# Kernel optimization log

Measured on AMD Instinct MI355X. Metric: run time of the kernel, lower is better.

The kernel has to match this reference:

```python
import jax, jax.numpy as jnp
import numpy as np

N, E = 50000, 800000
IN_DIM, H_DIM, OUT_DIM, EDGE_DIM, HEADS = 128, 128, 112, 8, 1
NEG_SLOPE = 0.2
BN_EPS = 1e-5


def _gat_layer(x, src, dst, edge_att, W, a_src, a_dst, We, a_edge, bias):
    """PyG GATConv (concat=False, edge_dim used for attention only)."""
    H, C = a_src.shape  # heads, out channels
    xs = (x @ W).reshape(-1, H, C)            # [N,H,C]
    ef = (edge_att @ We).reshape(-1, H, C)    # [E,H,C]
    al_src = jnp.einsum('nhc,hc->nh', xs, a_src)   # [N,H]
    al_dst = jnp.einsum('nhc,hc->nh', xs, a_dst)   # [N,H]
    al_edge = jnp.einsum('ehc,hc->eh', ef, a_edge) # [E,H]
    alpha = al_src[src] + al_dst[dst] + al_edge    # [E,H]
    alpha = jnp.where(alpha > 0, alpha, NEG_SLOPE * alpha)  # leaky_relu(0.2)
    # segment softmax over incoming edges of each dst node
    m = jax.lax.stop_gradient(jax.ops.segment_max(alpha, dst, num_segments=N))
    ex = jnp.exp(alpha - m[dst])
    den = jax.ops.segment_sum(ex, dst, num_segments=N)
    att = ex / den[dst]                       # [E,H]
    msg = xs[src] * att[:, :, None]           # [E,H,C] gather + weight
    out = jax.ops.segment_sum(msg, dst, num_segments=N)  # scatter-add [N,H,C]
    return out.mean(axis=1) + bias            # concat=False -> head mean


def _batchnorm(h, gamma, beta):
    mu = h.mean(axis=0)
    var = h.var(axis=0)
    return gamma * (h - mu) * jax.lax.rsqrt(var + BN_EPS) + beta


def setup_inputs() -> dict:
    key = jax.random.key(0)
    ks = jax.random.split(key, 20)
    s = 0.1
    inp = {
        'x': jax.random.normal(ks[0], (N, IN_DIM), dtype=jnp.float32),
        'edge_index': jax.random.randint(ks[1], (2, E), 0, N, dtype=jnp.int32),
        'edge_att': jax.random.normal(ks[2], (E, EDGE_DIM), dtype=jnp.float32),
        # layer 0: IN_DIM -> H_DIM
        'W0': s * jax.random.normal(ks[3], (IN_DIM, HEADS * H_DIM), dtype=jnp.float32),
        'a_src0': s * jax.random.normal(ks[4], (HEADS, H_DIM), dtype=jnp.float32),
        'a_dst0': s * jax.random.normal(ks[5], (HEADS, H_DIM), dtype=jnp.float32),
        'We0': s * jax.random.normal(ks[6], (EDGE_DIM, HEADS * H_DIM), dtype=jnp.float32),
        'a_edge0': s * jax.random.normal(ks[7], (HEADS, H_DIM), dtype=jnp.float32),
        'b0': jnp.zeros((H_DIM,), dtype=jnp.float32),
        # layer 1: H_DIM -> OUT_DIM
        'W1': s * jax.random.normal(ks[8], (H_DIM, HEADS * OUT_DIM), dtype=jnp.float32),
        'a_src1': s * jax.random.normal(ks[9], (HEADS, OUT_DIM), dtype=jnp.float32),
        'a_dst1': s * jax.random.normal(ks[10], (HEADS, OUT_DIM), dtype=jnp.float32),
        'We1': s * jax.random.normal(ks[11], (EDGE_DIM, HEADS * OUT_DIM), dtype=jnp.float32),
        'a_edge1': s * jax.random.normal(ks[12], (HEADS, OUT_DIM), dtype=jnp.float32),
        'b1': jnp.zeros((OUT_DIM,), dtype=jnp.float32),
        # batchnorms
        'bn_g': jnp.ones((H_DIM,), dtype=jnp.float32),
        'bn_b': jnp.zeros((H_DIM,), dtype=jnp.float32),
        'bnf_g': jnp.ones((OUT_DIM,), dtype=jnp.float32),
        'bnf_b': jnp.zeros((OUT_DIM,), dtype=jnp.float32),
    }
    return inp


def reference(x, edge_index, edge_att,
              W0, a_src0, a_dst0, We0, a_edge0, b0,
              W1, a_src1, a_dst1, We1, a_edge1, b1,
              bn_g, bn_b, bnf_g, bnf_b):
    src, dst = edge_index[0], edge_index[1]
    h = _gat_layer(x, src, dst, edge_att, W0, a_src0, a_dst0, We0, a_edge0, b0)
    h = _batchnorm(h, bn_g, bn_b)
    h = jax.nn.relu(h)
    # dropout is a no-op in eval; omitted for a deterministic reference
    h = _gat_layer(h, src, dst, edge_att, W1, a_src1, a_dst1, We1, a_edge1, b1)
    h = _batchnorm(h, bnf_g, bnf_b)
    return h
```

## Files before the change

kernel.cpp:

```cpp
#include <hip/hip_runtime.h>
#include <math.h>

#define NN 50000
#define NPAD 50048
#define NE 800000
#define SCAN_B 256
#define SCAN_NBLK ((NN + SCAN_B - 1) / SCAN_B)
#define AGG_NBLK 2048

typedef __attribute__((ext_vector_type(8))) short bf16x8;
typedef __attribute__((ext_vector_type(4))) float f32x4;
typedef __attribute__((ext_vector_type(8))) unsigned short u16x8;

__device__ __forceinline__ unsigned short f2bf(float x) {
    unsigned u = __float_as_uint(x);
    u += 0x7fffu + ((u >> 16) & 1);
    return (unsigned short)(u >> 16);
}
__device__ __forceinline__ float bf2f(unsigned short h) {
    return __uint_as_float(((unsigned)h) << 16);
}

__global__ void k_init_cvt(int* __restrict__ deg, float* __restrict__ stats,
                           const float* __restrict__ We0, const float* __restrict__ ae0,
                           const float* __restrict__ We1, const float* __restrict__ ae1,
                           float* __restrict__ ve,
                           const float* __restrict__ W0, const float* __restrict__ W1,
                           unsigned short* __restrict__ Wth0, unsigned short* __restrict__ Wtl0,
                           unsigned short* __restrict__ Wth1, unsigned short* __restrict__ Wtl1)
{
    int idx = blockIdx.x * 256 + threadIdx.x;
    if (idx < NN) deg[idx] = 0;
    if (idx < 512) stats[idx] = 0.f;
    if (idx < 128 * 128) {
        int k = idx / 128, c = idx % 128;
        float v = W0[idx];
        unsigned short hi = f2bf(v);
        Wth0[c * 128 + k] = hi;
        Wtl0[c * 128 + k] = f2bf(v - bf2f(hi));
    } else if (idx < 128 * 128 + 128 * 112) {
        int i2 = idx - 128 * 128;
        int k = i2 / 112, c = i2 % 112;
        float v = W1[i2];
        unsigned short hi = f2bf(v);
        Wth1[c * 128 + k] = hi;
        Wtl1[c * 128 + k] = f2bf(v - bf2f(hi));
    }
    if (blockIdx.x == gridDim.x - 1) {
        int j = threadIdx.x;
        if (j < 8) {
            float s = 0.f;
            for (int c = 0; c < 128; ++c) s += We0[j * 128 + c] * ae0[c];
            ve[j] = s;
        } else if (j < 16) {
            int jj = j - 8;
            float s = 0.f;
            for (int c = 0; c < 112; ++c) s += We1[jj * 112 + c] * ae1[c];
            ve[8 + jj] = s;
        }
    }
}

__global__ void k_deg(const int* __restrict__ dst, int* __restrict__ deg,
                      int* __restrict__ rank, int E_)
{
    int e = blockIdx.x * blockDim.x + threadIdx.x;
    if (e < E_) rank[e] = atomicAdd(&deg[dst[e]], 1);
}

__global__ void k_scan1(const int* __restrict__ deg, int* __restrict__ partial)
{
    __shared__ int sm[SCAN_B];
    int t = threadIdx.x;
    int idx = blockIdx.x * SCAN_B + t;
    sm[t] = (idx < NN) ? deg[idx] : 0;
    __syncthreads();
    #pragma unroll
    for (int off = SCAN_B / 2; off > 0; off >>= 1) {
        if (t < off) sm[t] += sm[t + off];
        __syncthreads();
    }
    if (t == 0) partial[blockIdx.x] = sm[0];
}

__global__ void k_scan3(const int* __restrict__ deg, const int* __restrict__ partial,
                        int* __restrict__ rp)
{
    __shared__ int sm[SCAN_B];
    __shared__ int pbase;
    int t = threadIdx.x;
    int pv = (t < SCAN_NBLK && t < blockIdx.x) ? partial[t] : 0;
    sm[t] = pv;
    __syncthreads();
    #pragma unroll
    for (int off = SCAN_B / 2; off > 0; off >>= 1) {
        if (t < off) sm[t] += sm[t + off];
        __syncthreads();
    }
    if (t == 0) pbase = sm[0];
    __syncthreads();
    int idx = blockIdx.x * SCAN_B + t;
    int v = (idx < NN) ? deg[idx] : 0;
    sm[t] = v;
    __syncthreads();
    #pragma unroll
    for (int off = 1; off < SCAN_B; off <<= 1) {
        int u = (t >= off) ? sm[t - off] : 0;
        __syncthreads();
        sm[t] += u;
        __syncthreads();
    }
    int excl = pbase + ((t == 0) ? 0 : sm[t - 1]);
    if (idx < NN) rp[idx] = excl;
    if (idx == NN - 1) rp[NN] = excl + v;
}

__global__ void k_csr_fill_l0(const int* __restrict__ src, const int* __restrict__ dst,
                              const float* __restrict__ eatt, const float* __restrict__ ve,
                              const int* __restrict__ rp, const int* __restrict__ rank,
                              const float* __restrict__ als, const float* __restrict__ ald,
                              uint4* __restrict__ pk, int E_)
{
    int e = blockIdx.x * blockDim.x + threadIdx.x;
    if (e >= E_) return;
    const float4* ea = reinterpret_cast<const float4*>(eatt + (size_t)e * 8);
    float4 e0 = ea[0], e1 = ea[1];
    float a0 = e0.x * ve[0] + e0.y * ve[1] + e0.z * ve[2] + e0.w * ve[3]
             + e1.x * ve[4] + e1.y * ve[5] + e1.z * ve[6] + e1.w * ve[7];
    float a1 = e0.x * ve[8] + e0.y * ve[9] + e0.z * ve[10] + e0.w * ve[11]
             + e1.x * ve[12] + e1.y * ve[13] + e1.z * ve[14] + e1.w * ve[15];
    int s = src[e], d = dst[e];
    float av = als[s] + ald[d] + a0;
    av = av > 0.f ? av : 0.2f * av;
    float ex0 = __expf(av);
    int pos = rp[d] + rank[e];
    uint4 rec;
    rec.x = (unsigned)s;
    rec.y = __float_as_uint(ex0);
    rec.z = __float_as_uint(a1);
    rec.w = 0u;
    pk[pos] = rec;
}

template<int COLS, bool BN_IN>
__launch_bounds__(256, 2)
__global__ void k_gemm_mfma(const float* __restrict__ A,
                            const unsigned short* __restrict__ Wth,
                            const unsigned short* __restrict__ Wtl,
                            unsigned short* __restrict__ out,
                            const float* __restrict__ a_src, const float* __restrict__ a_dst,
                            float* __restrict__ als, float* __restrict__ ald,
                            const float* __restrict__ bsum, const float* __restrict__ bsq,
                            const float* __restrict__ gamma, const float* __restrict__ beta)
{
    constexpr int NT = COLS / 16;
    __shared__ unsigned short sBh[COLS * 128];
    __shared__ unsigned short sBl[COLS * 128];
    __shared__ float scN[128], shN[128];

    int wv = threadIdx.x >> 6;
    int lane = threadIdx.x & 63;
    int r0 = blockIdx.x * 64 + wv * 16;
    int m = lane & 15;
    int quad = lane >> 4;
    int arow = r0 + m;
    int rc = (arow < NN) ? arow : NN - 1;
    const float* pa = A + (size_t)rc * 128 + quad * 8;

    float4 av[8];
    #pragma unroll
    for (int ks = 0; ks < 4; ++ks) {
        av[2 * ks]     = *reinterpret_cast<const float4*>(pa + ks * 32);
        av[2 * ks + 1] = *reinterpret_cast<const float4*>(pa + ks * 32 + 4);
    }

    constexpr int CH = COLS * 128 * 2 / 16;
    for (int i = threadIdx.x; i < CH; i += 256) {
        unsigned o = (unsigned)i * 16u;
        unsigned d = o ^ (((o >> 8) & 7u) << 4);
        *reinterpret_cast<uint4*>(reinterpret_cast<char*>(sBh) + d) =
            *reinterpret_cast<const uint4*>(reinterpret_cast<const char*>(Wth) + o);
        *reinterpret_cast<uint4*>(reinterpret_cast<char*>(sBl) + d) =
            *reinterpret_cast<const uint4*>(reinterpret_cast<const char*>(Wtl) + o);
    }
    if (BN_IN) {
        if (threadIdx.x < 128) {
            int k = threadIdx.x;
            float invn = 1.0f / (float)NN;
            float mean = bsum[k] * invn;
            float var  = bsq[k] * invn - mean * mean;
            float sc = gamma[k] * rsqrtf(var + 1e-5f);
            scN[k] = sc;
            shN[k] = beta[k] - mean * sc;
        }
    }
    __syncthreads();

    f32x4 acc[NT];
    #pragma unroll
    for (int t = 0; t < NT; ++t) acc[t] = f32x4{0.f, 0.f, 0.f, 0.f};

    unsigned swz = ((unsigned)(m & 7)) << 4;

    #pragma unroll
    for (int ks = 0; ks < 4; ++ks) {
        float4 v0 = av[2 * ks], v1 = av[2 * ks + 1];
        float vv[8] = {v0.x, v0.y, v0.z, v0.w, v1.x, v1.y, v1.z, v1.w};
        int kb = ks * 32 + quad * 8;
        bf16x8 ah, al;
        #pragma unroll
        for (int jj = 0; jj < 8; ++jj) {
            float f = vv[jj];
            if (BN_IN) f = fmaxf(f * scN[kb + jj] + shN[kb + jj], 0.f);
            unsigned short hi = f2bf(f);
            ah[jj] = (short)hi;
            al[jj] = (short)f2bf(f - bf2f(hi));
        }
        #pragma unroll
        for (int t = 0; t < NT; ++t) {
            int c = t * 16 + m;
            unsigned b = ((unsigned)c * 256u + (unsigned)ks * 64u + (unsigned)quad * 16u) ^ swz;
            bf16x8 bh = *reinterpret_cast<const bf16x8*>(reinterpret_cast<const char*>(sBh) + b);
            bf16x8 bl = *reinterpret_cast<const bf16x8*>(reinterpret_cast<const char*>(sBl) + b);
            acc[t] = __builtin_amdgcn_mfma_f32_16x16x32_bf16(ah, bh, acc[t], 0, 0, 0);
            acc[t] = __builtin_amdgcn_mfma_f32_16x16x32_bf16(al, bh, acc[t], 0, 0, 0);
            acc[t] = __builtin_amdgcn_mfma_f32_16x16x32_bf16(ah, bl, acc[t], 0, 0, 0);
        }
    }

    float p[4] = {0.f, 0.f, 0.f, 0.f}, q[4] = {0.f, 0.f, 0.f, 0.f};
    #pragma unroll
    for (int t = 0; t < NT; ++t) {
        int c = t * 16 + m;
        float asv = a_src[c], adv = a_dst[c];
        #pragma unroll
        for (int rI = 0; rI < 4; ++rI) {
            float v = acc[t][rI];
            int row = r0 + quad * 4 + rI;
            if (row < NN) out[(size_t)row * COLS + c] = f2bf(v);
            p[rI] += v * asv;
            q[rI] += v * adv;
        }
    }
    #pragma unroll
    for (int rI = 0; rI < 4; ++rI) {
        #pragma unroll
        for (int off = 1; off <= 8; off <<= 1) {
            p[rI] += __shfl_xor(p[rI], off);
            q[rI] += __shfl_xor(q[rI], off);
        }
    }
    if (m == 0) {
        #pragma unroll
        for (int rI = 0; rI < 4; ++rI) {
            int row = r0 + quad * 4 + rI;
            if (row < NN) { als[row] = p[rI]; ald[row] = q[rI]; }
        }
    }
}

__global__ void k_logit1(const int* __restrict__ rp, const uint4* __restrict__ pk,
                         const float* __restrict__ als, const float* __restrict__ ald,
                         uint2* __restrict__ pe)
{
    int ql = threadIdx.x & 15;
    int w = blockIdx.x * 16 + (threadIdx.x >> 4);
    if (w >= NN) return;
    int beg = rp[w], end = rp[w + 1];
    float aldv = ald[w];
    for (int p = beg + ql; p < end; p += 16) {
        uint4 r = pk[p];
        float a = als[r.x] + aldv + __uint_as_float(r.z);
        a = a > 0.f ? a : 0.2f * a;
        uint2 o;
        o.x = r.x;
        o.y = __float_as_uint(__expf(a));
        pe[p] = o;
    }
}

template<int COLS, int RSTRIDE>
__global__ void k_aggregate(const int* __restrict__ rp, const uint2* __restrict__ pe,
                            const unsigned short* __restrict__ xs, float* __restrict__ out,
                            float* __restrict__ psum, float* __restrict__ psq)
{
    __shared__ float sS[16 * 128], sQ[16 * 128];
    int ql = threadIdx.x & 15;
    int wq = threadIdx.x >> 4;
    int col = ql * 8;
    bool act = (col < COLS);
    int qid = blockIdx.x * 16 + wq;
    float bs[8] = {0.f,0.f,0.f,0.f,0.f,0.f,0.f,0.f};
    float bq[8] = {0.f,0.f,0.f,0.f,0.f,0.f,0.f,0.f};

    for (int w = qid; w < NN; w += AGG_NBLK * 16) {
        int beg = rp[w], end = rp[w + 1];
        float acc[8] = {0.f,0.f,0.f,0.f,0.f,0.f,0.f,0.f};
        float den = 0.f;
        int j = beg;
        for (; j + 4 <= end; j += 4) {
            uint2 r0 = pe[(size_t)(j    ) * RSTRIDE];
            uint2 r1 = pe[(size_t)(j + 1) * RSTRIDE];
            uint2 r2 = pe[(size_t)(j + 2) * RSTRIDE];
            uint2 r3 = pe[(size_t)(j + 3) * RSTRIDE];
            float e0 = __uint_as_float(r0.y);
            float e1 = __uint_as_float(r1.y);
            float e2 = __uint_as_float(r2.y);
            float e3 = __uint_as_float(r3.y);
            den += (e0 + e1) + (e2 + e3);
            if (act) {
                u16x8 u0 = *reinterpret_cast<const u16x8*>(xs + (size_t)r0.x * COLS + col);
                u16x8 u1 = *reinterpret_cast<const u16x8*>(xs + (size_t)r1.x * COLS + col);
                u16x8 u2 = *reinterpret_cast<const u16x8*>(xs + (size_t)r2.x * COLS + col);
                u16x8 u3 = *reinterpret_cast<const u16x8*>(xs + (size_t)r3.x * COLS + col);
                #pragma unroll
                for (int k = 0; k < 8; ++k)
                    acc[k] += (e0 * bf2f(u0[k]) + e1 * bf2f(u1[k]))
                            + (e2 * bf2f(u2[k]) + e3 * bf2f(u3[k]));
            }
        }
        if (j < end) {
            bool v1 = j + 1 < end;
            bool v2 = j + 2 < end;
            bool v3 = j + 3 < end;
            uint2 r0 = pe[(size_t)j * RSTRIDE];
            uint2 r1 = v1 ? pe[(size_t)(j + 1) * RSTRIDE] : uint2{0u, 0u};
            uint2 r2 = v2 ? pe[(size_t)(j + 2) * RSTRIDE] : uint2{0u, 0u};
            uint2 r3 = v3 ? pe[(size_t)(j + 3) * RSTRIDE] : uint2{0u, 0u};
            float e0 = __uint_as_float(r0.y);
            float e1 = __uint_as_float(r1.y);
            float e2 = __uint_as_float(r2.y);
            float e3 = __uint_as_float(r3.y);
            den += (e0 + e1) + (e2 + e3);
            if (act) {
                u16x8 u0 = *reinterpret_cast<const u16x8*>(xs + (size_t)r0.x * COLS + col);
                #pragma unroll
                for (int k = 0; k < 8; ++k) acc[k] += e0 * bf2f(u0[k]);
                if (v1) {
                    u16x8 u1 = *reinterpret_cast<const u16x8*>(xs + (size_t)r1.x * COLS + col);
                    #pragma unroll
                    for (int k = 0; k < 8; ++k) acc[k] += e1 * bf2f(u1[k]);
                }
                if (v2) {
                    u16x8 u2 = *reinterpret_cast<const u16x8*>(xs + (size_t)r2.x * COLS + col);
                    #pragma unroll
                    for (int k = 0; k < 8; ++k) acc[k] += e2 * bf2f(u2[k]);
                }
                if (v3) {
                    u16x8 u3 = *reinterpret_cast<const u16x8*>(xs + (size_t)r3.x * COLS + col);
                    #pragma unroll
                    for (int k = 0; k < 8; ++k) acc[k] += e3 * bf2f(u3[k]);
                }
            }
        }
        float inv = (end > beg) ? 1.f / den : 0.f;
        if (act) {
            float o[8];
            #pragma unroll
            for (int k = 0; k < 8; ++k) {
                o[k] = acc[k] * inv;
                bs[k] += o[k];
                bq[k] += o[k] * o[k];
            }
            f32x4 o0 = {o[0], o[1], o[2], o[3]};
            f32x4 o1 = {o[4], o[5], o[6], o[7]};
            __builtin_nontemporal_store(o0, reinterpret_cast<f32x4*>(out + (size_t)w * COLS + col));
            __builtin_nontemporal_store(o1, reinterpret_cast<f32x4*>(out + (size_t)w * COLS + col + 4));
        }
    }
    #pragma unroll
    for (int k = 0; k < 8; ++k) {
        sS[wq * 128 + col + k] = act ? bs[k] : 0.f;
        sQ[wq * 128 + col + k] = act ? bq[k] : 0.f;
    }
    __syncthreads();
    int t = threadIdx.x;
    if (t < 128) {
        float s = 0.f, s2 = 0.f;
        #pragma unroll
        for (int r = 0; r < 16; ++r) { s += sS[r * 128 + t]; s2 += sQ[r * 128 + t]; }
        psum[(size_t)blockIdx.x * 128 + t] = s;
        psq [(size_t)blockIdx.x * 128 + t] = s2;
    }
}

__global__ void k_bn_stats2(const float* __restrict__ psum, const float* __restrict__ psq,
                            float* __restrict__ sums, float* __restrict__ sqs)
{
    int t = threadIdx.x;
    int c = t & 127;
    constexpr int ROWS = AGG_NBLK / 128;
    const float* sp = (t < 128) ? psum : psq;
    float s = 0.f;
    #pragma unroll 4
    for (int i = 0; i < ROWS; ++i)
        s += sp[(size_t)(blockIdx.x * ROWS + i) * 128 + c];
    unsafeAtomicAdd(((t < 128) ? sums : sqs) + c, s);
}

template<int COLS>
__global__ void k_bn_apply(const float* __restrict__ in, float* __restrict__ out,
                           const float* __restrict__ sums, const float* __restrict__ sqs,
                           const float* __restrict__ gamma, const float* __restrict__ beta,
                           int n)
{
    int idx = blockIdx.x * blockDim.x + threadIdx.x;
    if (idx >= n * COLS) return;
    int c = idx % COLS;
    float invn = 1.0f / (float)n;
    float mean = sums[c] * invn;
    float var  = sqs[c] * invn - mean * mean;
    float sc = gamma[c] * rsqrtf(var + 1e-5f);
    float sh = beta[c] - mean * sc;
    out[idx] = in[idx] * sc + sh;
}

extern "C" void kernel_launch(void* const* d_in, const int* in_sizes, int n_in,
                              void* d_out, int out_size, void* d_ws, size_t ws_size,
                              hipStream_t stream)
{
    const float* x    = (const float*)d_in[0];
    const int*   eidx = (const int*)d_in[1];
    const float* eatt = (const float*)d_in[2];
    const float* W0   = (const float*)d_in[3];
    const float* as0  = (const float*)d_in[4];
    const float* ad0  = (const float*)d_in[5];
    const float* We0  = (const float*)d_in[6];
    const float* ae0  = (const float*)d_in[7];
    const float* W1   = (const float*)d_in[9];
    const float* as1  = (const float*)d_in[10];
    const float* ad1  = (const float*)d_in[11];
    const float* We1  = (const float*)d_in[12];
    const float* ae1  = (const float*)d_in[13];
    const float* bng  = (const float*)d_in[15];
    const float* bnb  = (const float*)d_in[16];
    const float* bnfg = (const float*)d_in[17];
    const float* bnfb = (const float*)d_in[18];

    const int N = NN, E = NE;
    const int* src = eidx;
    const int* dst = eidx + E;

    float* ws = (float*)d_ws;
    size_t off = 0;
    unsigned short* xs0b = (unsigned short*)(ws + off); off += (size_t)N * 64;
    float* h   = ws + off;      off += (size_t)N * 128;
    unsigned short* xs1b = (unsigned short*)(ws + off); off += (size_t)N * 56;
    int*   rp   = (int*)(ws + off);     off += N + 2;
    int*   rank = (int*)(ws + off);     off += E;
    int*   deg  = (int*)(ws + off);     off += N;
    float* als0 = ws + off;     off += N;
    float* ald0 = ws + off;     off += N;
    float* als1 = ws + off;     off += N;
    float* ald1 = ws + off;     off += N;
    float* stats = ws + off;    off += 512;
    float* ve = ws + off;       off += 16;
    int*   partial = (int*)(ws + off);  off += SCAN_NBLK;
    float* psum = ws + off;     off += (size_t)AGG_NBLK * 128;
    float* psq  = ws + off;     off += (size_t)AGG_NBLK * 128;
    unsigned short* Wth0 = (unsigned short*)(ws + off); off += 128 * 64;
    unsigned short* Wtl0 = (unsigned short*)(ws + off); off += 128 * 64;
    unsigned short* Wth1 = (unsigned short*)(ws + off); off += 112 * 64;
    unsigned short* Wtl1 = (unsigned short*)(ws + off); off += 112 * 64;
    float* out1 = h;

    uint4* pk  = (uint4*)d_out;
    uint2* pe1 = (uint2*)((char*)d_out + (size_t)E * 16);

    float* sum0 = stats;
    float* sq0  = stats + 128;
    float* sum1 = stats + 256;
    float* sq1  = stats + 384;

    k_init_cvt<<<(N + 255) / 256, 256, 0, stream>>>(deg, stats, We0, ae0, We1, ae1, ve,
                                                    W0, W1, Wth0, Wtl0, Wth1, Wtl1);

    k_deg<<<(E + 255) / 256, 256, 0, stream>>>(dst, deg, rank, E);
    k_scan1<<<SCAN_NBLK, SCAN_B, 0, stream>>>(deg, partial);
    k_scan3<<<SCAN_NBLK, SCAN_B, 0, stream>>>(deg, partial, rp);

    k_gemm_mfma<128, false><<<NPAD / 64, 256, 0, stream>>>(x, Wth0, Wtl0, xs0b,
                                                           as0, ad0, als0, ald0,
                                                           nullptr, nullptr, nullptr, nullptr);
    k_csr_fill_l0<<<(E + 255) / 256, 256, 0, stream>>>(src, dst, eatt, ve, rp, rank,
                                                       als0, ald0, pk, E);
    k_aggregate<128, 2><<<AGG_NBLK, 256, 0, stream>>>(rp, (const uint2*)pk, xs0b, h, psum, psq);
    k_bn_stats2<<<128, 256, 0, stream>>>(psum, psq, sum0, sq0);

    k_gemm_mfma<112, true><<<NPAD / 64, 256, 0, stream>>>(h, Wth1, Wtl1, xs1b,
                                                          as1, ad1, als1, ald1,
                                                          sum0, sq0, bng, bnb);
    k_logit1<<<(N + 15) / 16, 256, 0, stream>>>(rp, pk, als1, ald1, pe1);
    k_aggregate<112, 1><<<AGG_NBLK, 256, 0, stream>>>(rp, pe1, xs1b, out1, psum, psq);
    k_bn_stats2<<<128, 256, 0, stream>>>(psum, psq, sum1, sq1);
    k_bn_apply<112><<<(N * 112 + 255) / 256, 256, 0, stream>>>(out1, (float*)d_out, sum1, sq1, bnfg, bnfb, N);
}
```

Baseline: 339.8 us.

## Pack edge records into 8 bytes and unroll aggregation by eight

Each CSR edge record shrinks from a 16-byte uint4 to an 8-byte uint2. The source index goes in the low 16 bits, the layer-1 edge logit as bf16 in the high 16 bits, and the exp value in the second word. The fill kernel now handles two edges per thread with vectorized index loads. The aggregate kernel is unrolled to eight edges per iteration and now reads a contiguous record stream. The aggregate block count goes up, and rank/deg/pe1 are aliased onto workspace buffers that are already dead, so scratch no longer lives in the output buffer. This cuts scatter and gather bytes, but relies on N fitting in 16 bits and stores the edge logit at bf16 precision.

Measured after the change: 345.9 us. About the same (+1.8%).

```diff
diff --git a/kernel.cpp b/kernel.cpp
--- a/kernel.cpp
+++ b/kernel.cpp
@@ -6,7 +6,7 @@
 #define NE 800000
 #define SCAN_B 256
 #define SCAN_NBLK ((NN + SCAN_B - 1) / SCAN_B)
-#define AGG_NBLK 2048
+#define AGG_NBLK 3200
 
 typedef __attribute__((ext_vector_type(8))) short bf16x8;
 typedef __attribute__((ext_vector_type(4))) float f32x4;
@@ -119,27 +119,40 @@
                               const float* __restrict__ eatt, const float* __restrict__ ve,
                               const int* __restrict__ rp, const int* __restrict__ rank,
                               const float* __restrict__ als, const float* __restrict__ ald,
-                              uint4* __restrict__ pk, int E_)
-{
-    int e = blockIdx.x * blockDim.x + threadIdx.x;
+                              uint2* __restrict__ pk, int E_)
+{
+    int i = blockIdx.x * blockDim.x + threadIdx.x;
+    int e = i * 2;
     if (e >= E_) return;
+    int2 ss = *reinterpret_cast<const int2*>(src + e);
+    int2 dd = *reinterpret_cast<const int2*>(dst + e);
+    int2 rr = *reinterpret_cast<const int2*>(rank + e);
     const float4* ea = reinterpret_cast<const float4*>(eatt + (size_t)e * 8);
-    float4 e0 = ea[0], e1 = ea[1];
-    float a0 = e0.x * ve[0] + e0.y * ve[1] + e0.z * ve[2] + e0.w * ve[3]
-             + e1.x * ve[4] + e1.y * ve[5] + e1.z * ve[6] + e1.w * ve[7];
-    float a1 = e0.x * ve[8] + e0.y * ve[9] + e0.z * ve[10] + e0.w * ve[11]
-             + e1.x * ve[12] + e1.y * ve[13] + e1.z * ve[14] + e1.w * ve[15];
-    int s = src[e], d = dst[e];
-    float av = als[s] + ald[d] + a0;
-    av = av > 0.f ? av : 0.2f * av;
-    float ex0 = __expf(av);
-    int pos = rp[d] + rank[e];
-    uint4 rec;
-    rec.x = (unsigned)s;
-    rec.y = __float_as_uint(ex0);
-    rec.z = __float_as_uint(a1);
-    rec.w = 0u;
-    pk[pos] = rec;
+    float4 ea0 = ea[0], ea1 = ea[1], ea2 = ea[2], ea3 = ea[3];
+
+    float a0x = ea0.x * ve[0] + ea0.y * ve[1] + ea0.z * ve[2] + ea0.w * ve[3]
+              + ea1.x * ve[4] + ea1.y * ve[5] + ea1.z * ve[6] + ea1.w * ve[7];
+    float a1x = ea0.x * ve[8] + ea0.y * ve[9] + ea0.z * ve[10] + ea0.w * ve[11]
+              + ea1.x * ve[12] + ea1.y * ve[13] + ea1.z * ve[14] + ea1.w * ve[15];
+    float a0y = ea2.x * ve[0] + ea2.y * ve[1] + ea2.z * ve[2] + ea2.w * ve[3]
+              + ea3.x * ve[4] + ea3.y * ve[5] + ea3.z * ve[6] + ea3.w * ve[7];
+    float a1y = ea2.x * ve[8] + ea2.y * ve[9] + ea2.z * ve[10] + ea2.w * ve[11]
+              + ea3.x * ve[12] + ea3.y * ve[13] + ea3.z * ve[14] + ea3.w * ve[15];
+
+    int p0 = rp[dd.x] + rr.x;
+    int p1 = rp[dd.y] + rr.y;
+    float lx = als[ss.x] + ald[dd.x] + a0x;
+    float ly = als[ss.y] + ald[dd.y] + a0y;
+    lx = lx > 0.f ? lx : 0.2f * lx;
+    ly = ly > 0.f ? ly : 0.2f * ly;
+
+    uint2 r0, r1;
+    r0.x = (unsigned)ss.x | ((unsigned)f2bf(a1x) << 16);
+    r0.y = __float_as_uint(__expf(lx));
+    r1.x = (unsigned)ss.y | ((unsigned)f2bf(a1y) << 16);
+    r1.y = __float_as_uint(__expf(ly));
+    pk[p0] = r0;
+    pk[p1] = r1;
 }
 
 template<int COLS, bool BN_IN>
@@ -259,9 +272,9 @@
     }
 }
 
-__global__ void k_logit1(const int* __restrict__ rp, const uint4* __restrict__ pk,
+__global__ void k_logit1(const int* __restrict__ rp, const uint2* __restrict__ pk,
                          const float* __restrict__ als, const float* __restrict__ ald,
-                         uint2* __restrict__ pe)
+                         uint2* __restrict__ pe1)
 {
     int ql = threadIdx.x & 15;
     int w = blockIdx.x * 16 + (threadIdx.x >> 4);
@@ -269,17 +282,17 @@
     int beg = rp[w], end = rp[w + 1];
     float aldv = ald[w];
     for (int p = beg + ql; p < end; p += 16) {
-        uint4 r = pk[p];
-        float a = als[r.x] + aldv + __uint_as_float(r.z);
+        uint2 r = pk[p];
+        float a = als[r.x & 0xffffu] + aldv + bf2f((unsigned short)(r.x >> 16));
         a = a > 0.f ? a : 0.2f * a;
         uint2 o;
         o.x = r.x;
         o.y = __float_as_uint(__expf(a));
-        pe[p] = o;
-    }
-}
-
-template<int COLS, int RSTRIDE>
+        pe1[p] = o;
+    }
+}
+
+template<int COLS>
 __global__ void k_aggregate(const int* __restrict__ rp, const uint2* __restrict__ pe,
                             const unsigned short* __restrict__ xs, float* __restrict__ out,
                             float* __restrict__ psum, float* __restrict__ psq)
@@ -298,58 +311,79 @@
         float acc[8] = {0.f,0.f,0.f,0.f,0.f,0.f,0.f,0.f};
         float den = 0.f;
         int j = beg;
-        for (; j + 4 <= end; j += 4) {
-            uint2 r0 = pe[(size_t)(j    ) * RSTRIDE];
-            uint2 r1 = pe[(size_t)(j + 1) * RSTRIDE];
-            uint2 r2 = pe[(size_t)(j + 2) * RSTRIDE];
-            uint2 r3 = pe[(size_t)(j + 3) * RSTRIDE];
-            float e0 = __uint_as_float(r0.y);
-            float e1 = __uint_as_float(r1.y);
-            float e2 = __uint_as_float(r2.y);
-            float e3 = __uint_as_float(r3.y);
-            den += (e0 + e1) + (e2 + e3);
+        for (; j + 8 <= end; j += 8) {
+            uint2 r0 = pe[j],     r1 = pe[j + 1], r2 = pe[j + 2], r3 = pe[j + 3];
+            uint2 r4 = pe[j + 4], r5 = pe[j + 5], r6 = pe[j + 6], r7 = pe[j + 7];
+            float e0 = __uint_as_float(r0.y), e1 = __uint_as_float(r1.y);
+            float e2 = __uint_as_float(r2.y), e3 = __uint_as_float(r3.y);
+            float e4 = __uint_as_float(r4.y), e5 = __uint_as_float(r5.y);
+            float e6 = __uint_as_float(r6.y), e7 = __uint_as_float(r7.y);
+            den += ((e0 + e1) + (e2 + e3)) + ((e4 + e5) + (e6 + e7));
             if (act) {
-                u16x8 u0 = *reinterpret_cast<const u16x8*>(xs + (size_t)r0.x * COLS + col);
-                u16x8 u1 = *reinterpret_cast<const u16x8*>(xs + (size_t)r1.x * COLS + col);
-                u16x8 u2 = *reinterpret_cast<const u16x8*>(xs + (size_t)r2.x * COLS + col);
-                u16x8 u3 = *reinterpret_cast<const u16x8*>(xs + (size_t)r3.x * COLS + col);
+                u16x8 u0 = *reinterpret_cast<const u16x8*>(xs + (size_t)(r0.x & 0xffffu) * COLS + col);
+                u16x8 u1 = *reinterpret_cast<const u16x8*>(xs + (size_t)(r1.x & 0xffffu) * COLS + col);
+                u16x8 u2 = *reinterpret_cast<const u16x8*>(xs + (size_t)(r2.x & 0xffffu) * COLS + col);
+                u16x8 u3 = *reinterpret_cast<const u16x8*>(xs + (size_t)(r3.x & 0xffffu) * COLS + col);
+                u16x8 u4 = *reinterpret_cast<const u16x8*>(xs + (size_t)(r4.x & 0xffffu) * COLS + col);
+                u16x8 u5 = *reinterpret_cast<const u16x8*>(xs + (size_t)(r5.x & 0xffffu) * COLS + col);
+                u16x8 u6 = *reinterpret_cast<const u16x8*>(xs + (size_t)(r6.x & 0xffffu) * COLS + col);
+                u16x8 u7 = *reinterpret_cast<const u16x8*>(xs + (size_t)(r7.x & 0xffffu) * COLS + col);
                 #pragma unroll
                 for (int k = 0; k < 8; ++k)
-                    acc[k] += (e0 * bf2f(u0[k]) + e1 * bf2f(u1[k]))
-                            + (e2 * bf2f(u2[k]) + e3 * bf2f(u3[k]));
+                    acc[k] += (((e0 * bf2f(u0[k]) + e1 * bf2f(u1[k]))
+                              + (e2 * bf2f(u2[k]) + e3 * bf2f(u3[k])))
+                             + ((e4 * bf2f(u4[k]) + e5 * bf2f(u5[k]))
+                              + (e6 * bf2f(u6[k]) + e7 * bf2f(u7[k]))));
             }
         }
         if (j < end) {
-            bool v1 = j + 1 < end;
-            bool v2 = j + 2 < end;
-            bool v3 = j + 3 < end;
-            uint2 r0 = pe[(size_t)j * RSTRIDE];
-            uint2 r1 = v1 ? pe[(size_t)(j + 1) * RSTRIDE] : uint2{0u, 0u};
-            uint2 r2 = v2 ? pe[(size_t)(j + 2) * RSTRIDE] : uint2{0u, 0u};
-            uint2 r3 = v3 ? pe[(size_t)(j + 3) * RSTRIDE] : uint2{0u, 0u};
-            float e0 = __uint_as_float(r0.y);
-            float e1 = __uint_as_float(r1.y);
-            float e2 = __uint_as_float(r2.y);
-            float e3 = __uint_as_float(r3.y);
-            den += (e0 + e1) + (e2 + e3);
+            bool v1 = j + 1 < end, v2 = j + 2 < end, v3 = j + 3 < end;
+            bool v4 = j + 4 < end, v5 = j + 5 < end, v6 = j + 6 < end;
+            uint2 r0 = pe[j];
+            uint2 r1 = v1 ? pe[j + 1] : uint2{0u, 0u};
+            uint2 r2 = v2 ? pe[j + 2] : uint2{0u, 0u};
+            uint2 r3 = v3 ? pe[j + 3] : uint2{0u, 0u};
+            uint2 r4 = v4 ? pe[j + 4] : uint2{0u, 0u};
+            uint2 r5 = v5 ? pe[j + 5] : uint2{0u, 0u};
+            uint2 r6 = v6 ? pe[j + 6] : uint2{0u, 0u};
+            float e0 = __uint_as_float(r0.y), e1 = __uint_as_float(r1.y);
+            float e2 = __uint_as_float(r2.y), e3 = __uint_as_float(r3.y);
+            float e4 = __uint_as_float(r4.y), e5 = __uint_as_float(r5.y);
+            float e6 = __uint_as_float(r6.y);
+            den += ((e0 + e1) + (e2 + e3)) + ((e4 + e5) + e6);
             if (act) {
-                u16x8 u0 = *reinterpret_cast<const u16x8*>(xs + (size_t)r0.x * COLS + col);
+                u16x8 u0 = *reinterpret_cast<const u16x8*>(xs + (size_t)(r0.x & 0xffffu) * COLS + col);
                 #pragma unroll
                 for (int k = 0; k < 8; ++k) acc[k] += e0 * bf2f(u0[k]);
                 if (v1) {
-                    u16x8 u1 = *reinterpret_cast<const u16x8*>(xs + (size_t)r1.x * COLS + col);
+                    u16x8 u = *reinterpret_cast<const u16x8*>(xs + (size_t)(r1.x & 0xffffu) * COLS + col);
                     #pragma unroll
-                    for (int k = 0; k < 8; ++k) acc[k] += e1 * bf2f(u1[k]);
+                    for (int k = 0; k < 8; ++k) acc[k] += e1 * bf2f(u[k]);
                 }
                 if (v2) {
-                    u16x8 u2 = *reinterpret_cast<const u16x8*>(xs + (size_t)r2.x * COLS + col);
+                    u16x8 u = *reinterpret_cast<const u16x8*>(xs + (size_t)(r2.x & 0xffffu) * COLS + col);
                     #pragma unroll
-                    for (int k = 0; k < 8; ++k) acc[k] += e2 * bf2f(u2[k]);
+                    for (int k = 0; k < 8; ++k) acc[k] += e2 * bf2f(u[k]);
                 }
                 if (v3) {
-                    u16x8 u3 = *reinterpret_cast<const u16x8*>(xs + (size_t)r3.x * COLS + col);
+                    u16x8 u = *reinterpret_cast<const u16x8*>(xs + (size_t)(r3.x & 0xffffu) * COLS + col);
                     #pragma unroll
-                    for (int k = 0; k < 8; ++k) acc[k] += e3 * bf2f(u3[k]);
+                    for (int k = 0; k < 8; ++k) acc[k] += e3 * bf2f(u[k]);
+                }
+                if (v4) {
+                    u16x8 u = *reinterpret_cast<const u16x8*>(xs + (size_t)(r4.x & 0xffffu) * COLS + col);
+                    #pragma unroll
+                    for (int k = 0; k < 8; ++k) acc[k] += e4 * bf2f(u[k]);
+                }
+                if (v5) {
+                    u16x8 u = *reinterpret_cast<const u16x8*>(xs + (size_t)(r5.x & 0xffffu) * COLS + col);
+                    #pragma unroll
+                    for (int k = 0; k < 8; ++k) acc[k] += e5 * bf2f(u[k]);
+                }
+                if (v6) {
+                    u16x8 u = *reinterpret_cast<const u16x8*>(xs + (size_t)(r6.x & 0xffffu) * COLS + col);
+                    #pragma unroll
+                    for (int k = 0; k < 8; ++k) acc[k] += e6 * bf2f(u[k]);
                 }
             }
         }
@@ -392,7 +426,7 @@
     constexpr int ROWS = AGG_NBLK / 128;
     const float* sp = (t < 128) ? psum : psq;
     float s = 0.f;
-    #pragma unroll 4
+    #pragma unroll 5
     for (int i = 0; i < ROWS; ++i)
         s += sp[(size_t)(blockIdx.x * ROWS + i) * 128 + c];
     unsafeAtomicAdd(((t < 128) ? sums : sqs) + c, s);
@@ -446,9 +480,8 @@
     unsigned short* xs0b = (unsigned short*)(ws + off); off += (size_t)N * 64;
     float* h   = ws + off;      off += (size_t)N * 128;
     unsigned short* xs1b = (unsigned short*)(ws + off); off += (size_t)N * 56;
+    uint2* pk = (uint2*)(ws + off);     off += (size_t)E * 2;
     int*   rp   = (int*)(ws + off);     off += N + 2;
-    int*   rank = (int*)(ws + off);     off += E;
-    int*   deg  = (int*)(ws + off);     off += N;
     float* als0 = ws + off;     off += N;
     float* ald0 = ws + off;     off += N;
     float* als1 = ws + off;     off += N;
@@ -462,10 +495,11 @@
     unsigned short* Wtl0 = (unsigned short*)(ws + off); off += 128 * 64;
     unsigned short* Wth1 = (unsigned short*)(ws + off); off += 112 * 64;
     unsigned short* Wtl1 = (unsigned short*)(ws + off); off += 112 * 64;
+
+    int*   rank = (int*)h;
+    int*   deg  = (int*)(h + 800000);
+    uint2* pe1  = (uint2*)xs0b;
     float* out1 = h;
-
-    uint4* pk  = (uint4*)d_out;
-    uint2* pe1 = (uint2*)((char*)d_out + (size_t)E * 16);
 
     float* sum0 = stats;
     float* sq0  = stats + 128;
@@ -482,16 +516,16 @@
     k_gemm_mfma<128, false><<<NPAD / 64, 256, 0, stream>>>(x, Wth0, Wtl0, xs0b,
                                                            as0, ad0, als0, ald0,
                                                            nullptr, nullptr, nullptr, nullptr);
-    k_csr_fill_l0<<<(E + 255) / 256, 256, 0, stream>>>(src, dst, eatt, ve, rp, rank,
-                                                       als0, ald0, pk, E);
-    k_aggregate<128, 2><<<AGG_NBLK, 256, 0, stream>>>(rp, (const uint2*)pk, xs0b, h, psum, psq);
+    k_csr_fill_l0<<<(E / 2 + 255) / 256, 256, 0, stream>>>(src, dst, eatt, ve, rp, rank,
+                                                           als0, ald0, pk, E);
+    k_aggregate<128><<<AGG_NBLK, 256, 0, stream>>>(rp, pk, xs0b, h, psum, psq);
     k_bn_stats2<<<128, 256, 0, stream>>>(psum, psq, sum0, sq0);
 
     k_gemm_mfma<112, true><<<NPAD / 64, 256, 0, stream>>>(h, Wth1, Wtl1, xs1b,
                                                           as1, ad1, als1, ald1,
                                                           sum0, sq0, bng, bnb);
     k_logit1<<<(N + 15) / 16, 256, 0, stream>>>(rp, pk, als1, ald1, pe1);
-    k_aggregate<112, 1><<<AGG_NBLK, 256, 0, stream>>>(rp, pe1, xs1b, out1, psum, psq);
+    k_aggregate<112><<<AGG_NBLK, 256, 0, stream>>>(rp, pe1, xs1b, out1, psum, psq);
     k_bn_stats2<<<128, 256, 0, stream>>>(psum, psq, sum1, sq1);
     k_bn_apply<112><<<(N * 112 + 255) / 256, 256, 0, stream>>>(out1, (float*)d_out, sum1, sq1, bnfg, bnfb, N);
 }
```
